# Kernel tuning notes

Measured on AMD Instinct MI355X. Metric: run time of the kernel, lower is better.

The kernel has to match this reference:

```python
import jax, jax.numpy as jnp
import numpy as np

B, S, D, H = 2, 2048, 1024, 16
DK = D // H


def setup_inputs() -> dict:
    key = jax.random.key(0)
    ks = jax.random.split(key, 12)
    scale = 1.0 / np.sqrt(D)
    inp = {
        "pre_Q": jax.random.normal(ks[0], (B, S, D), jnp.float32),
        "pre_K": jax.random.normal(ks[1], (B, S, D), jnp.float32),
        "pre_V": jax.random.normal(ks[2], (B, S, D), jnp.float32),
        "Wq": jax.random.normal(ks[3], (D, D), jnp.float32) * scale,
        "bq": jnp.zeros((D,), jnp.float32),
        "Wk": jax.random.normal(ks[4], (D, D), jnp.float32) * scale,
        "bk": jnp.zeros((D,), jnp.float32),
        "Wv": jax.random.normal(ks[5], (D, D), jnp.float32) * scale,
        "bv": jnp.zeros((D,), jnp.float32),
        "Wo": jax.random.normal(ks[6], (D, D), jnp.float32) * scale,
        "bo": jnp.zeros((D,), jnp.float32),
        "mask": jnp.ones((B, 1, 1, S), jnp.int32),
    }
    return inp


def _split_heads(x):
    # (B, S, D) -> (B, H, S, DK)
    return x.reshape(B, S, H, DK).transpose(0, 2, 1, 3)


def reference(pre_Q, pre_K, pre_V, Wq, bq, Wk, bk, Wv, bv, Wo, bo, mask):
    # linear projections (torch nn.Linear: x @ W.T + b)
    Q = _split_heads(pre_Q @ Wq.T + bq)
    K = _split_heads(pre_K @ Wk.T + bk)
    V = _split_heads(pre_V @ Wv.T + bv)
    # scaled dot-product attention; dropout is identity in eval mode
    scores = jnp.einsum("bhqd,bhkd->bhqk", Q, K) / np.sqrt(DK).astype(np.float32)
    scores = jnp.where(mask == 0, jnp.float32(-1e9), scores)
    weights = jax.nn.softmax(scores, axis=-1)
    ctx = jnp.einsum("bhqk,bhkd->bhqd", weights, V)  # (B, H, S, DK)
    concat = ctx.transpose(0, 2, 1, 3).reshape(B, S, D)
    return concat @ Wo.T + bo
```

## Files before the change

kernel.cpp:

```cpp
#include <hip/hip_runtime.h>

#define SS 2048
#define DD 1024
#define HH 16
#define MM 4096
#define KK 1024

typedef __attribute__((ext_vector_type(8))) short bf16x8;
typedef __attribute__((ext_vector_type(4))) float f32x4;
typedef __attribute__((ext_vector_type(16))) float f32x16;
typedef __attribute__((ext_vector_type(4))) float float4_t;
typedef __attribute__((ext_vector_type(4))) short short4_t;

__device__ __forceinline__ short f2bf(float f) {
    union { float f; unsigned u; } x; x.f = f;
    unsigned r = x.u + 0x7fffu + ((x.u >> 16) & 1u);
    return (short)(r >> 16);
}
__device__ __forceinline__ float bf2f(short s) {
    union { unsigned u; float f; } x; x.u = ((unsigned)(unsigned short)s) << 16;
    return x.f;
}

__device__ __forceinline__ f32x4 mfma16(bf16x8 a, bf16x8 b, f32x4 c) {
    return __builtin_amdgcn_mfma_f32_16x16x32_bf16(a, b, c, 0, 0, 0);
}
__device__ __forceinline__ f32x16 mfma32(bf16x8 a, bf16x8 b, f32x16 c) {
    return __builtin_amdgcn_mfma_f32_32x32x16_bf16(a, b, c, 0, 0, 0);
}

__device__ __forceinline__ void gl_lds16(const void* g, void* l) {
    __builtin_amdgcn_global_load_lds(
        (const __attribute__((address_space(1))) void*)g,
        (__attribute__((address_space(3))) void*)l, 16, 0, 0);
}

__device__ __forceinline__ float exp2a(float x) {
    float r; asm("v_exp_f32 %0, %1" : "=v"(r) : "v"(x)); return r;
}
__device__ __forceinline__ int cvtpk(float lo, float hi) {
    int r; asm("v_cvt_pk_bf16_f32 %0, %1, %2" : "=v"(r) : "v"(lo), "v"(hi)); return r;
}
__device__ __forceinline__ void pswap(int& a, int& b) {
    asm("v_permlane32_swap_b32 %0, %1" : "+v"(a), "+v"(b));
}

__global__ __launch_bounds__(256)
void conv_all(const float* __restrict__ x0, const float* __restrict__ x1,
              const float* __restrict__ x2,
              const float* __restrict__ w0, const float* __restrict__ w1,
              const float* __restrict__ w2, const float* __restrict__ w3,
              short* __restrict__ Xb, short* __restrict__ Wb) {
    const int bid = blockIdx.x;
    const float* src;
    short* dst;
    size_t i;
    if (bid < 6144) {
        const int plane = bid >> 11, idx = bid & 2047;
        src = (plane == 0) ? x0 : (plane == 1) ? x1 : x2;
        i = ((size_t)idx * 256 + threadIdx.x) * 8;
        dst = Xb + (size_t)plane * MM * KK;
    } else {
        const int b2 = bid - 6144;
        const int plane = b2 >> 9, idx = b2 & 511;
        src = (plane == 0) ? w0 : (plane == 1) ? w1 : (plane == 2) ? w2 : w3;
        i = ((size_t)idx * 256 + threadIdx.x) * 8;
        dst = Wb + (size_t)plane * KK * KK;
    }
    float4_t a = *(const float4_t*)(src + i);
    float4_t b = *(const float4_t*)(src + i + 4);
    bf16x8 o;
#pragma unroll
    for (int e = 0; e < 4; ++e) { o[e] = f2bf(a[e]); o[4 + e] = f2bf(b[e]); }
    *(bf16x8*)(dst + i) = o;
}

template <int NI>
__device__ __forceinline__ void gemm_core(const short* __restrict__ A,
                                          const short* __restrict__ Bw,
                                          int m0, int n0,
                                          char* As, char* Bs,
                                          f32x4 acc[4][NI]) {
    const int tid = threadIdx.x;
    const int lane = tid & 63, w = tid >> 6;
    const int wr = w >> 1, wc = w & 1;

    const short* srcA[4];
#pragma unroll
    for (int jj = 0; jj < 4; ++jj) {
        const int c = tid + jj * 256;
        const int arow = ((c >> 9) << 6) + (((c >> 7) & 3) << 4) + (c & 15);
        const int akc  = (((c >> 6) & 1) << 2) + ((c >> 4) & 3);
        srcA[jj] = A + (size_t)(m0 + arow) * KK + akc * 8;
    }
    const short* srcB[NI];
#pragma unroll
    for (int jj = 0; jj < NI; ++jj) {
        const int c = tid + jj * 256;
        const int wcb = c / (NI * 128), rem = c % (NI * 128);
        const int brow = wcb * (16 * NI) + ((rem >> 7) << 4) + (c & 15);
        const int bkc  = (((c >> 6) & 1) << 2) + ((c >> 4) & 3);
        srcB[jj] = Bw + (size_t)(n0 + brow) * KK + bkc * 8;
    }
    char* ldA = As + tid * 16;
    char* ldB = Bs + tid * 16;
    constexpr int ABYTES = 16384;
    constexpr int BBYTES = NI * 4096;

#define GSTAGE(buf, kofs)                                                   \
    { _Pragma("unroll")                                                     \
      for (int jj = 0; jj < 4; ++jj)                                        \
          gl_lds16(srcA[jj] + (kofs), ldA + (buf) * ABYTES + jj * 4096);    \
      _Pragma("unroll")                                                     \
      for (int jj = 0; jj < NI; ++jj)                                       \
          gl_lds16(srcB[jj] + (kofs), ldB + (buf) * BBYTES + jj * 4096); }

    GSTAGE(0, 0);
    __syncthreads();
    int cur = 0;
    const int Ab = wr * 8192 + lane * 16;
    const int Bb = wc * (NI * 2048) + lane * 16;
    for (int kt = 0; kt < KK / 64; ++kt) {
        if (kt + 1 < KK / 64) GSTAGE(cur ^ 1, (kt + 1) * 64);
        const char* ba = As + cur * ABYTES + Ab;
        const char* bb = Bs + cur * BBYTES + Bb;
#pragma unroll
        for (int ks = 0; ks < 2; ++ks) {
            bf16x8 af[4], bfr[NI];
#pragma unroll
            for (int i = 0; i < 4; ++i)
                af[i] = *(const bf16x8*)(ba + i * 2048 + ks * 1024);
#pragma unroll
            for (int ni = 0; ni < NI; ++ni)
                bfr[ni] = *(const bf16x8*)(bb + ni * 2048 + ks * 1024);
#pragma unroll
            for (int mi = 0; mi < 4; ++mi)
#pragma unroll
                for (int ni = 0; ni < NI; ++ni)
                    acc[mi][ni] = mfma16(af[mi], bfr[ni], acc[mi][ni]);
        }
        __syncthreads();
        cur ^= 1;
    }
#undef GSTAGE
}

__global__ __launch_bounds__(256, 2)
void qkv_gemm(const short* __restrict__ Xb, const short* __restrict__ Wb,
              const float* __restrict__ bq, const float* __restrict__ bk,
              const float* __restrict__ bv,
              short* __restrict__ Qo, short* __restrict__ Ko, short* __restrict__ Vto) {
    __shared__ __align__(16) char As[2 * 16384];
    __shared__ __align__(16) char Bs[2 * 16384];
    const int z = blockIdx.z;
    const short* A = Xb + (size_t)z * MM * KK;
    const short* W = Wb + (size_t)z * KK * KK;
    const float* bias = (z == 0) ? bq : (z == 1) ? bk : bv;
    const float scale = (z == 0) ? 0.125f * 1.44269504088896f : 1.0f;
    const int m0 = blockIdx.x * 128, n0 = blockIdx.y * 128;

    f32x4 zero = {0.f, 0.f, 0.f, 0.f};
    f32x4 acc[4][4];
#pragma unroll
    for (int i = 0; i < 4; ++i)
#pragma unroll
        for (int j = 0; j < 4; ++j) acc[i][j] = zero;

    gemm_core<4>(A, W, m0, n0, As, Bs, acc);

    const int tid = threadIdx.x;
    const int lane = tid & 63, w = tid >> 6;
    const int wr = w >> 1, wc = w & 1;
    const int lr = lane & 15, lg = lane >> 4;

#pragma unroll
    for (int mi = 0; mi < 4; ++mi) {
        const int mbase = m0 + wr * 64 + mi * 16 + lg * 4;
        const int b = mbase >> 11, s = mbase & 2047;
#pragma unroll
        for (int ni = 0; ni < 4; ++ni) {
            const int n = n0 + wc * 64 + ni * 16 + lr;
            const float bvv = bias[n];
            const int h = n >> 6, dk = n & 63;
            if (z == 2) {
                short4_t pk;
#pragma unroll
                for (int r = 0; r < 4; ++r) pk[r] = f2bf(acc[mi][ni][r] + bvv);
                *(short4_t*)(Vto + ((size_t)((b * HH + h) * 64 + dk) << 11) + s) = pk;
            } else {
                short* dst = (z == 0) ? Qo : Ko;
#pragma unroll
                for (int r = 0; r < 4; ++r)
                    dst[((size_t)((b * HH + h) * SS + (s + r)) << 6) + dk] =
                        f2bf((acc[mi][ni][r] + bvv) * scale);
            }
        }
    }
}

__global__ __launch_bounds__(256, 2)
void out_gemm(const short* __restrict__ ctx, const short* __restrict__ Wo,
              const float* __restrict__ bo, float* __restrict__ out) {
    __shared__ __align__(16) char As[2 * 16384];
    __shared__ __align__(16) char Bs[2 * 8192];
    const int m0 = blockIdx.x * 128, n0 = blockIdx.y * 64;

    f32x4 zero = {0.f, 0.f, 0.f, 0.f};
    f32x4 acc[4][2];
#pragma unroll
    for (int i = 0; i < 4; ++i)
#pragma unroll
        for (int j = 0; j < 2; ++j) acc[i][j] = zero;

    gemm_core<2>(ctx, Wo, m0, n0, As, Bs, acc);

    const int tid = threadIdx.x;
    const int lane = tid & 63, w = tid >> 6;
    const int wr = w >> 1, wc = w & 1;
    const int lr = lane & 15, lg = lane >> 4;

#pragma unroll
    for (int mi = 0; mi < 4; ++mi)
#pragma unroll
        for (int ni = 0; ni < 2; ++ni) {
            const int n = n0 + wc * 32 + ni * 16 + lr;
            const float bvv = bo[n];
#pragma unroll
            for (int r = 0; r < 4; ++r) {
                const int m = m0 + wr * 64 + mi * 16 + lg * 4 + r;
                out[(size_t)m * KK + n] = acc[mi][ni][r] + bvv;
            }
        }
}

__global__ __launch_bounds__(256, 4)
void attn_kernel(const short* __restrict__ Qg, const short* __restrict__ Kg,
                 const short* __restrict__ Vtg, const int* __restrict__ mask,
                 short* __restrict__ Po, float* __restrict__ Pm, float* __restrict__ Pl) {
    __shared__ __align__(16) short Ks[2][4096];
    __shared__ __align__(16) short Vs[2][4096];

    const int tid = threadIdx.x, w = tid >> 6, lane = tid & 63;
    const int l31 = lane & 31, hi = lane >> 5;
    const int bh = blockIdx.y, b = bh >> 4;
    const int half = blockIdx.z;
    const int q0w = blockIdx.x * 128 + w * 32;

    const short* Qh = Qg + (size_t)bh * SS * 64;
    const short* Kh = Kg + (size_t)bh * SS * 64;
    const short* Vh = Vtg + (size_t)bh * 64 * SS;
    const int* mrow = mask + b * SS;

    bf16x8 qf[4];
#pragma unroll
    for (int t = 0; t < 4; ++t)
        qf[t] = *(const bf16x8*)(Qh + (q0w + l31) * 64 + t * 16 + hi * 8);

    f32x16 octx0, octx1;
#pragma unroll
    for (int r = 0; r < 16; ++r) { octx0[r] = 0.f; octx1[r] = 0.f; }
    float mrun = -1e30f, lrun = 0.f;

    const int tq = (tid >> 6) & 3;
    const short* gk0 = Kh + (l31) * 64 + tq * 16 + hi * 8;
    const short* gk1 = Kh + (32 + l31) * 64 + tq * 16 + hi * 8;
    const short* gv0 = Vh + (size_t)(l31) * SS + tq * 16 + hi * 8;
    const short* gv1 = Vh + (size_t)(32 + l31) * SS + tq * 16 + hi * 8;
    char* lK = (char*)Ks + tid * 16;
    char* lV = (char*)Vs + tid * 16;

#define ASTAGE(buf, key0)                                      \
    { gl_lds16(gk0 + (key0) * 64, lK + (buf) * 8192);          \
      gl_lds16(gk1 + (key0) * 64, lK + 4096 + (buf) * 8192);   \
      gl_lds16(gv0 + (key0), lV + (buf) * 8192);               \
      gl_lds16(gv1 + (key0), lV + 4096 + (buf) * 8192); }

    const int it0 = half * (SS / 128), it1 = it0 + (SS / 128);
    ASTAGE(0, it0 * 64);
    __syncthreads();
    int cur = 0;

    for (int it = it0; it < it1; ++it) {
        const int key0 = it * 64;
        if (it + 1 < it1) ASTAGE(cur ^ 1, key0 + 64);

        const char* cK = (const char*)Ks + cur * 8192;
        const char* cV = (const char*)Vs + cur * 8192;

        f32x16 s0, s1;
#pragma unroll
        for (int r = 0; r < 16; ++r) { s0[r] = 0.f; s1[r] = 0.f; }
#pragma unroll
        for (int t = 0; t < 4; ++t) {
            bf16x8 a0 = *(const bf16x8*)(cK + ((0 * 4 + t) * 64 + lane) * 16);
            bf16x8 a1 = *(const bf16x8*)(cK + ((1 * 4 + t) * 64 + lane) * 16);
            s0 = mfma32(a0, qf[t], s0);
            s1 = mfma32(a1, qf[t], s1);
        }

        const int mk = mrow[key0 + lane];
        if (!__all(mk != 0)) {
#pragma unroll
            for (int r = 0; r < 16; ++r) {
                const int kl = (r & 3) + 8 * (r >> 2) + 4 * hi;
                if (mrow[key0 + kl] == 0) s0[r] = -1e9f;
                if (mrow[key0 + 32 + kl] == 0) s1[r] = -1e9f;
            }
        }

        float tv[16];
#pragma unroll
        for (int r = 0; r < 16; ++r) tv[r] = fmaxf(s0[r], s1[r]);
#pragma unroll
        for (int off = 8; off >= 1; off >>= 1)
#pragma unroll
            for (int r = 0; r < 8; ++r)
                if (r < off) tv[r] = fmaxf(tv[r], tv[r + off]);
        float tm = tv[0];
        tm = fmaxf(tm, __shfl_xor(tm, 32));

        if (!__all(tm <= mrun + 8.0f)) {
            const float mnew = fmaxf(mrun, tm);
            const float alpha = exp2a(mrun - mnew);
            lrun *= alpha;
#pragma unroll
            for (int r = 0; r < 16; ++r) {
                const int ql = (r & 3) + 8 * (r >> 2) + 4 * hi;
                const float aq = __shfl(alpha, ql);
                octx0[r] *= aq;
                octx1[r] *= aq;
            }
            mrun = mnew;
        }

#pragma unroll
        for (int r = 0; r < 16; ++r) {
            s0[r] = exp2a(s0[r] - mrun);
            s1[r] = exp2a(s1[r] - mrun);
        }
        float sv[16];
#pragma unroll
        for (int r = 0; r < 16; ++r) sv[r] = s0[r] + s1[r];
#pragma unroll
        for (int off = 8; off >= 1; off >>= 1)
#pragma unroll
            for (int r = 0; r < 8; ++r)
                if (r < off) sv[r] += sv[r + off];
        float rs = sv[0];
        rs += __shfl_xor(rs, 32);
        lrun += rs;

        bf16x8 pa[4];
#pragma unroll
        for (int kb = 0; kb < 2; ++kb) {
            const f32x16& sv16 = kb ? s1 : s0;
#pragma unroll
            for (int halfp = 0; halfp < 2; ++halfp) {
                const int base = halfp * 8;
                int A  = cvtpk(sv16[base + 0], sv16[base + 1]);
                int Bw = cvtpk(sv16[base + 2], sv16[base + 3]);
                int Cw = cvtpk(sv16[base + 4], sv16[base + 5]);
                int Dw = cvtpk(sv16[base + 6], sv16[base + 7]);
                pswap(A, Cw);
                pswap(Bw, Dw);
                union { int wv[4]; bf16x8 v; } u;
                u.wv[0] = A; u.wv[1] = Bw; u.wv[2] = Cw; u.wv[3] = Dw;
                pa[kb * 2 + halfp] = u.v;
            }
        }

#pragma unroll
        for (int kk = 0; kk < 4; ++kk) {
            bf16x8 v0 = *(const bf16x8*)(cV + ((0 * 4 + kk) * 64 + lane) * 16);
            bf16x8 v1 = *(const bf16x8*)(cV + ((1 * 4 + kk) * 64 + lane) * 16);
            octx0 = mfma32(pa[kk], v0, octx0);
            octx1 = mfma32(pa[kk], v1, octx1);
        }

        __syncthreads();
        cur ^= 1;
    }
#undef ASTAGE

    const size_t pbase = (size_t)(half * 32 + bh) * SS;
#pragma unroll
    for (int r = 0; r < 16; ++r) {
        const int ql = (r & 3) + 8 * (r >> 2) + 4 * hi;
        short* prow = Po + (pbase + q0w + ql) * 64 + l31;
        prow[0]  = f2bf(octx0[r]);
        prow[32] = f2bf(octx1[r]);
    }
    if (hi == 0) {
        Pm[pbase + q0w + l31] = mrun;
        Pl[pbase + q0w + l31] = lrun;
    }
}

__global__ __launch_bounds__(256)
void attn_combine(const short* __restrict__ Po, const float* __restrict__ Pm,
                  const float* __restrict__ Pl, short* __restrict__ ctxb) {
    const int idx = blockIdx.x * 256 + threadIdx.x;
    const int d0 = (idx & 7) * 8;
    const int s  = (idx >> 3) & (SS - 1);
    const int bh = idx >> 14;
    const int b = bh >> 4, h = bh & 15;

    const size_t i1 = (size_t)bh * SS + s;
    const size_t i2 = (size_t)(32 + bh) * SS + s;
    const float m1 = Pm[i1], m2 = Pm[i2];
    const float l1 = Pl[i1], l2 = Pl[i2];
    const float m = fmaxf(m1, m2);
    const float w1 = exp2a(m1 - m), w2 = exp2a(m2 - m);
    const float inv = 1.f / (l1 * w1 + l2 * w2);

    bf16x8 o1 = *(const bf16x8*)(Po + i1 * 64 + d0);
    bf16x8 o2 = *(const bf16x8*)(Po + i2 * 64 + d0);
    bf16x8 o;
#pragma unroll
    for (int j = 0; j < 8; ++j)
        o[j] = f2bf((bf2f(o1[j]) * w1 + bf2f(o2[j]) * w2) * inv);
    *(bf16x8*)(ctxb + ((size_t)(b * SS + s)) * DD + h * 64 + d0) = o;
}

extern "C" void kernel_launch(void* const* d_in, const int* in_sizes, int n_in,
                              void* d_out, int out_size, void* d_ws, size_t ws_size,
                              hipStream_t stream) {
    const float* preQ = (const float*)d_in[0];
    const float* preK = (const float*)d_in[1];
    const float* preV = (const float*)d_in[2];
    const float* Wq   = (const float*)d_in[3];
    const float* bq   = (const float*)d_in[4];
    const float* Wk   = (const float*)d_in[5];
    const float* bk   = (const float*)d_in[6];
    const float* Wv   = (const float*)d_in[7];
    const float* bv   = (const float*)d_in[8];
    const float* Wo   = (const float*)d_in[9];
    const float* bo   = (const float*)d_in[10];
    const int*   mask = (const int*)d_in[11];
    float* out = (float*)d_out;

    char* ws = (char*)d_ws;
    short* Xb  = (short*)(ws);
    short* Wb  = (short*)(ws + (size_t)25165824);
    short* Qw  = (short*)(ws + (size_t)33554432);
    short* Kw  = (short*)(ws + (size_t)41943040);
    short* Vtw = (short*)(ws + (size_t)50331648);
    short* Ctx = (short*)(ws + (size_t)58720256);
    short* Po  = (short*)(ws + (size_t)67108864);
    float* Pm  = (float*)(ws + (size_t)83886080);
    float* Pl  = (float*)(ws + (size_t)84410368);

    conv_all<<<dim3(8192), 256, 0, stream>>>(preQ, preK, preV, Wq, Wk, Wv, Wo, Xb, Wb);
    qkv_gemm<<<dim3(32, 8, 3), 256, 0, stream>>>(Xb, Wb, bq, bk, bv, Qw, Kw, Vtw);
    attn_kernel<<<dim3(16, 32, 2), 256, 0, stream>>>(Qw, Kw, Vtw, mask, Po, Pm, Pl);
    attn_combine<<<dim3(2048), 256, 0, stream>>>(Po, Pm, Pl, Ctx);
    out_gemm<<<dim3(32, 16), 256, 0, stream>>>(Ctx, Wb + (size_t)3 * KK * KK, bo, out);
}
```

Before: 270.6 us.

## Shrink GEMM K-tile to 32 with XOR-swizzled row-major LDS layout and higher occupancy

The shared GEMM core now stages 32-wide K tiles instead of 64 into a row-major LDS layout. Chunk indices are XOR-swizzled to avoid bank conflicts, which replaces the old pre-permuted fragment layout. Halving LDS per block lets launch bounds ask for 4 blocks per CU instead of 2, hiding memory latency with more resident waves. The cost is twice as many K iterations and barriers per tile, plus tighter register pressure under the higher occupancy bound.

```diff
diff --git a/kernel.cpp b/kernel.cpp
--- a/kernel.cpp
+++ b/kernel.cpp
@@ -84,74 +84,60 @@
     const int tid = threadIdx.x;
     const int lane = tid & 63, w = tid >> 6;
     const int wr = w >> 1, wc = w & 1;
-
-    const short* srcA[4];
-#pragma unroll
-    for (int jj = 0; jj < 4; ++jj) {
-        const int c = tid + jj * 256;
-        const int arow = ((c >> 9) << 6) + (((c >> 7) & 3) << 4) + (c & 15);
-        const int akc  = (((c >> 6) & 1) << 2) + ((c >> 4) & 3);
-        srcA[jj] = A + (size_t)(m0 + arow) * KK + akc * 8;
-    }
-    const short* srcB[NI];
-#pragma unroll
-    for (int jj = 0; jj < NI; ++jj) {
-        const int c = tid + jj * 256;
-        const int wcb = c / (NI * 128), rem = c % (NI * 128);
-        const int brow = wcb * (16 * NI) + ((rem >> 7) << 4) + (c & 15);
-        const int bkc  = (((c >> 6) & 1) << 2) + ((c >> 4) & 3);
-        srcB[jj] = Bw + (size_t)(n0 + brow) * KK + bkc * 8;
-    }
-    char* ldA = As + tid * 16;
-    char* ldB = Bs + tid * 16;
-    constexpr int ABYTES = 16384;
-    constexpr int BBYTES = NI * 4096;
-
-#define GSTAGE(buf, kofs)                                                   \
-    { _Pragma("unroll")                                                     \
-      for (int jj = 0; jj < 4; ++jj)                                        \
-          gl_lds16(srcA[jj] + (kofs), ldA + (buf) * ABYTES + jj * 4096);    \
-      _Pragma("unroll")                                                     \
-      for (int jj = 0; jj < NI; ++jj)                                       \
-          gl_lds16(srcB[jj] + (kofs), ldB + (buf) * BBYTES + jj * 4096); }
+    const int lr = lane & 15, lg = lane >> 4;
+
+    const int rA = tid >> 2;
+    const int kcA = (tid & 3) ^ ((rA >> 1) & 3);
+    const short* ga0 = A + (size_t)(m0 + rA) * KK + kcA * 8;
+    const short* ga1 = ga0 + (size_t)64 * KK;
+    const short* gb0 = Bw + (size_t)(n0 + rA) * KK + kcA * 8;
+    const short* gb1 = gb0 + (size_t)64 * KK;
+    char* lA = As + tid * 16;
+    char* lB = Bs + tid * 16;
+    constexpr int BBUF = NI * 2048;
+
+#define GSTAGE(buf, kofs)                                        \
+    { gl_lds16(ga0 + (kofs), lA + (buf) * 8192);                 \
+      gl_lds16(ga1 + (kofs), lA + 4096 + (buf) * 8192);          \
+      gl_lds16(gb0 + (kofs), lB + (buf) * BBUF);                 \
+      if constexpr (NI == 4)                                     \
+          gl_lds16(gb1 + (kofs), lB + 4096 + (buf) * BBUF); }
 
     GSTAGE(0, 0);
     __syncthreads();
     int cur = 0;
-    const int Ab = wr * 8192 + lane * 16;
-    const int Bb = wc * (NI * 2048) + lane * 16;
-    for (int kt = 0; kt < KK / 64; ++kt) {
-        if (kt + 1 < KK / 64) GSTAGE(cur ^ 1, (kt + 1) * 64);
-        const char* ba = As + cur * ABYTES + Ab;
-        const char* bb = Bs + cur * BBYTES + Bb;
-#pragma unroll
-        for (int ks = 0; ks < 2; ++ks) {
-            bf16x8 af[4], bfr[NI];
-#pragma unroll
-            for (int i = 0; i < 4; ++i)
-                af[i] = *(const bf16x8*)(ba + i * 2048 + ks * 1024);
+    const int swz = ((lr >> 1) & 3) * 16;
+    const int aoff = (wr * 64 + lr) * 64 + (lg * 16 ^ swz);
+    const int boff = (wc * (NI * 16) + lr) * 64 + (lg * 16 ^ swz);
+    for (int kt = 0; kt < KK / 32; ++kt) {
+        if (kt + 1 < KK / 32) GSTAGE(cur ^ 1, (kt + 1) * 32);
+        const char* ba = As + cur * 8192 + aoff;
+        const char* bb = Bs + cur * BBUF + boff;
+        bf16x8 af[4], bfr[NI];
+#pragma unroll
+        for (int i = 0; i < 4; ++i)
+            af[i] = *(const bf16x8*)(ba + i * 1024);
+#pragma unroll
+        for (int ni = 0; ni < NI; ++ni)
+            bfr[ni] = *(const bf16x8*)(bb + ni * 1024);
+#pragma unroll
+        for (int mi = 0; mi < 4; ++mi)
 #pragma unroll
             for (int ni = 0; ni < NI; ++ni)
-                bfr[ni] = *(const bf16x8*)(bb + ni * 2048 + ks * 1024);
-#pragma unroll
-            for (int mi = 0; mi < 4; ++mi)
-#pragma unroll
-                for (int ni = 0; ni < NI; ++ni)
-                    acc[mi][ni] = mfma16(af[mi], bfr[ni], acc[mi][ni]);
-        }
+                acc[mi][ni] = mfma16(af[mi], bfr[ni], acc[mi][ni]);
         __syncthreads();
         cur ^= 1;
     }
 #undef GSTAGE
 }
 
-__global__ __launch_bounds__(256, 2)
+__global__ __launch_bounds__(256, 4)
 void qkv_gemm(const short* __restrict__ Xb, const short* __restrict__ Wb,
               const float* __restrict__ bq, const float* __restrict__ bk,
               const float* __restrict__ bv,
               short* __restrict__ Qo, short* __restrict__ Ko, short* __restrict__ Vto) {
-    __shared__ __align__(16) char As[2 * 16384];
-    __shared__ __align__(16) char Bs[2 * 16384];
+    __shared__ __align__(16) char As[2 * 8192];
+    __shared__ __align__(16) char Bs[2 * 8192];
     const int z = blockIdx.z;
     const short* A = Xb + (size_t)z * MM * KK;
     const short* W = Wb + (size_t)z * KK * KK;
@@ -198,11 +184,11 @@
     }
 }
 
-__global__ __launch_bounds__(256, 2)
+__global__ __launch_bounds__(256, 4)
 void out_gemm(const short* __restrict__ ctx, const short* __restrict__ Wo,
               const float* __restrict__ bo, float* __restrict__ out) {
-    __shared__ __align__(16) char As[2 * 16384];
-    __shared__ __align__(16) char Bs[2 * 8192];
+    __shared__ __align__(16) char As[2 * 8192];
+    __shared__ __align__(16) char Bs[2 * 4096];
     const int m0 = blockIdx.x * 128, n0 = blockIdx.y * 64;
 
     f32x4 zero = {0.f, 0.f, 0.f, 0.f};
```

After: 236.1 us. -12.8%, faster.
